# Optimization experiments

Measured on AMD Instinct MI355X. Metric: run time of the kernel, lower is better.

The kernel has to match this reference:

```python
import math
import jax, jax.numpy as jnp
import numpy as np

FACTOR = 5
HEAD_DIM = 64  # hard-coded in the original reshape


def setup_inputs() -> dict:
    key = jax.random.key(0)
    kq, kk, kv, ki = jax.random.split(key, 4)
    B, L, H, D = 16, 4096, 8, HEAD_DIM
    S = 4096
    u = FACTOR * math.ceil(math.log(L))  # sample_k = 45
    return {
        "queries": jax.random.normal(kq, (B, L, H, D), dtype=jnp.float32),
        "keys": jax.random.normal(kk, (B, S, H, D), dtype=jnp.float32),
        "values": jax.random.normal(kv, (B, S, H, D), dtype=jnp.float32),
        "sample_idx": jax.random.randint(ki, (u,), 0, S, dtype=jnp.int32),
    }


def reference(queries, keys, values, sample_idx):
    B, L, H, D = queries.shape
    S = keys.shape[1]
    # faithful to tf.reshape (memory reinterpret), not a transpose
    Q = queries.reshape(B, H, L, HEAD_DIM)
    K = keys.reshape(B, H, S, HEAD_DIM)
    V = values.reshape(B, H, S, HEAD_DIM)

    U = FACTOR * math.ceil(math.log(S))  # n_top queries kept

    # --- _prob_QK (without materializing K_expand: sampled keys are shared
    # across all query positions) ---
    K_sample = K[:, :, sample_idx, :]                      # [B,H,u,64]
    Q_K_sample = jnp.einsum('bhld,bhkd->bhlk', Q, K_sample)  # [B,H,L,u]
    # sparsity measure: max - mean (divided by full key length S)
    M = Q_K_sample.max(axis=-1) - Q_K_sample.sum(axis=-1) / S  # [B,H,L]
    _, M_top = jax.lax.top_k(M, U)                          # [B,H,U]

    Q_reduce = jnp.take_along_axis(Q, M_top[..., None], axis=2)  # [B,H,U,64]
    scores = jnp.einsum('bhud,bhsd->bhus', Q_reduce, K)          # [B,H,U,S]

    scale = 1.0 / math.sqrt(HEAD_DIM)
    scores = scores * scale

    # --- initial context: sum of V broadcast over all query positions ---
    V_sum = V.sum(axis=-2)                                  # [B,H,64]
    context = jnp.broadcast_to(V_sum[:, :, None, :], (B, H, L, HEAD_DIM))

    # --- update rows of the top-U queries with real attention output ---
    attn = jax.nn.softmax(scores, axis=-1)                  # [B,H,U,S]
    top_ctx = jnp.einsum('bhus,bhsd->bhud', attn, V)        # [B,H,U,64]

    b_idx = jnp.arange(B)[:, None, None]
    h_idx = jnp.arange(H)[None, :, None]
    context = context.at[b_idx, h_idx, M_top].set(top_ctx)
    return context
```

## Files before the change

### kernel.cpp

```cpp
#include <hip/hip_runtime.h>
#include <hip/hip_bf16.h>
#include <math.h>

#define NBH 128
#define LQ  4096
#define SK  4096
#define DH  64
#define NS  45
#define TOPSTRIDE 48
#define NCH 8
#define CK  512

typedef __attribute__((ext_vector_type(8))) short short8v;
typedef __attribute__((ext_vector_type(4))) short short4v;
typedef __attribute__((ext_vector_type(4))) float f32x4;

static __device__ __forceinline__ short f2b(float x) {
    union { __hip_bfloat16 h; short s; } u;
    u.h = __float2bfloat16(x);
    return u.s;
}
static __device__ __forceinline__ short8v cvt8(const float* p) {
    float4 a = *(const float4*)p, b = *(const float4*)(p + 4);
    short8v r;
    r[0]=f2b(a.x); r[1]=f2b(a.y); r[2]=f2b(a.z); r[3]=f2b(a.w);
    r[4]=f2b(b.x); r[5]=f2b(b.y); r[6]=f2b(b.z); r[7]=f2b(b.w);
    return r;
}
static __device__ __forceinline__ f32x4 mfma16(short4v a, short4v b, f32x4 c) {
#if __has_builtin(__builtin_amdgcn_mfma_f32_16x16x16bf16_1k)
    return __builtin_amdgcn_mfma_f32_16x16x16bf16_1k(a, b, c, 0, 0, 0);
#else
    asm volatile("v_mfma_f32_16x16x16_bf16 %0, %1, %2, %0" : "+v"(c) : "v"(a), "v"(b));
    return c;
#endif
}

__global__ __launch_bounds__(256) void kernelM(const float* __restrict__ Q,
                                               const float* __restrict__ K,
                                               const int* __restrict__ sidx,
                                               float* __restrict__ M) {
    __shared__ __attribute__((aligned(16))) float Ks[NS][DH];
    const int bh = blockIdx.x >> 4;
    const int qb = (blockIdx.x & 15) << 8;
    for (int i = threadIdx.x; i < NS * 16; i += 256) {
        int k = i >> 4, f4 = i & 15;
        *(float4*)&Ks[k][f4 * 4] =
            *(const float4*)(K + ((size_t)bh * SK + sidx[k]) * DH + f4 * 4);
    }
    __syncthreads();
    const int q = qb + threadIdx.x;
    const float* qp = Q + (((size_t)bh << 12) + q) * DH;
    float qr[DH];
#pragma unroll
    for (int i = 0; i < 16; i++) {
        float4 v = *(const float4*)(qp + 4 * i);
        qr[4*i] = v.x; qr[4*i+1] = v.y; qr[4*i+2] = v.z; qr[4*i+3] = v.w;
    }
    float vmax = -INFINITY, vsum = 0.f;
#pragma unroll 3
    for (int k = 0; k < NS; k++) {
        float d0 = 0.f, d1 = 0.f, d2 = 0.f, d3 = 0.f;
#pragma unroll
        for (int j = 0; j < 16; j++) {
            float4 kv = *(const float4*)&Ks[k][4 * j];
            d0 += qr[4*j+0] * kv.x;
            d1 += qr[4*j+1] * kv.y;
            d2 += qr[4*j+2] * kv.z;
            d3 += qr[4*j+3] * kv.w;
        }
        float dot = (d0 + d1) + (d2 + d3);
        vmax = fmaxf(vmax, dot);
        vsum += dot;
    }
    M[((size_t)bh << 12) + q] = vmax - vsum * (1.0f / 4096.0f);
}

__global__ __launch_bounds__(256) void kernelTopK(const float* __restrict__ M,
                                                  int* __restrict__ top) {
    __shared__ float m[LQ];
    __shared__ float rv[256];
    __shared__ int   ri[256];
    int bh = blockIdx.x;
    for (int i = threadIdx.x; i < LQ; i += 256) m[i] = M[((size_t)bh << 12) + i];
    __syncthreads();
    for (int it = 0; it < NS; ++it) {
        float bv = -INFINITY; int bi = 0x7fffffff;
        for (int i = threadIdx.x; i < LQ; i += 256) {
            float v = m[i];
            if (v > bv) { bv = v; bi = i; }
        }
        rv[threadIdx.x] = bv; ri[threadIdx.x] = bi;
        __syncthreads();
        for (int s = 128; s; s >>= 1) {
            if (threadIdx.x < s) {
                float ov = rv[threadIdx.x + s]; int oi = ri[threadIdx.x + s];
                if (ov > rv[threadIdx.x] || (ov == rv[threadIdx.x] && oi < ri[threadIdx.x])) {
                    rv[threadIdx.x] = ov; ri[threadIdx.x] = oi;
                }
            }
            __syncthreads();
        }
        if (threadIdx.x == 0) { top[bh * TOPSTRIDE + it] = ri[0]; m[ri[0]] = -INFINITY; }
        __syncthreads();
    }
}

__global__ __launch_bounds__(256) void kernelAttn2(const float* __restrict__ Q,
                                                   const float* __restrict__ K,
                                                   const float* __restrict__ V,
                                                   const int* __restrict__ top,
                                                   float* __restrict__ pm,
                                                   float* __restrict__ pl,
                                                   float* __restrict__ pacc,
                                                   float* __restrict__ vsum) {
    __shared__ float lm[4][48];
    __shared__ float ll[4][48];
    __shared__ __attribute__((aligned(16))) float ob[48][68];

    const int bh = blockIdx.x >> 3, c = blockIdx.x & 7;
    const int tid = threadIdx.x, w = tid >> 6, l = tid & 63;
    const int b = l >> 4, n = l & 15;
    const int kwavebase = c * CK + w * 128;
    const size_t bhoff = ((size_t)bh << 12) * DH;

    const int* topb = top + bh * TOPSTRIDE;
    short8v qf[3][2];
#pragma unroll
    for (int qt = 0; qt < 3; qt++) {
        int q = qt * 16 + n;
        int row = topb[q < NS ? q : NS - 1];
        const float* qp = Q + bhoff + (size_t)row * DH;
#pragma unroll
        for (int t = 0; t < 2; t++) qf[qt][t] = cvt8(qp + 32 * t + 8 * b);
    }

    f32x4 o[3][4];
    float m_run[3], l_run[3], vacc[4];
#pragma unroll
    for (int qt = 0; qt < 3; qt++) {
        m_run[qt] = -INFINITY; l_run[qt] = 0.f;
#pragma unroll
        for (int dt = 0; dt < 4; dt++) { o[qt][dt][0]=0.f; o[qt][dt][1]=0.f; o[qt][dt][2]=0.f; o[qt][dt][3]=0.f; }
    }
#pragma unroll
    for (int dt = 0; dt < 4; dt++) vacc[dt] = 0.f;

    for (int s = 0; s < 8; ++s) {
        const float* kp = K + bhoff + (size_t)(kwavebase + s * 16 + n) * DH;
        short8v ka0 = cvt8(kp + 8 * b);
        short8v ka1 = cvt8(kp + 32 + 8 * b);
        const float* vp = V + bhoff + (size_t)(kwavebase + s * 16 + 4 * b) * DH;
        short4v vb[4];
#pragma unroll
        for (int dt = 0; dt < 4; dt++) {
            float v0 = vp[0 * DH + dt * 16 + n];
            float v1 = vp[1 * DH + dt * 16 + n];
            float v2 = vp[2 * DH + dt * 16 + n];
            float v3 = vp[3 * DH + dt * 16 + n];
            vacc[dt] += (v0 + v1) + (v2 + v3);
            short4v vv; vv[0]=f2b(v0); vv[1]=f2b(v1); vv[2]=f2b(v2); vv[3]=f2b(v3);
            vb[dt] = vv;
        }
        f32x4 st[3];
        float mnew[3];
        bool need = false;
#pragma unroll
        for (int qt = 0; qt < 3; qt++) {
            f32x4 acc0 = {0.f, 0.f, 0.f, 0.f};
            acc0 = __builtin_amdgcn_mfma_f32_16x16x32_bf16(ka0, qf[qt][0], acc0, 0, 0, 0);
            acc0 = __builtin_amdgcn_mfma_f32_16x16x32_bf16(ka1, qf[qt][1], acc0, 0, 0, 0);
            acc0 = acc0 * 0.125f;
            st[qt] = acc0;
            float tm = fmaxf(fmaxf(acc0[0], acc0[1]), fmaxf(acc0[2], acc0[3]));
            tm = fmaxf(tm, __shfl_xor(tm, 16, 64));
            tm = fmaxf(tm, __shfl_xor(tm, 32, 64));
            mnew[qt] = fmaxf(m_run[qt], tm);
            need = need || (mnew[qt] > m_run[qt]);
        }
        if (__any(need)) {
            float rl[3];
#pragma unroll
            for (int qt = 0; qt < 3; qt++) {
                rl[qt] = __expf(m_run[qt] - mnew[qt]);
                l_run[qt] *= rl[qt];
            }
#pragma unroll
            for (int qt = 0; qt < 3; qt++) {
#pragma unroll
                for (int rr = 0; rr < 4; rr++) {
                    float rs = __shfl(rl[qt], 20 * b + rr, 64);
#pragma unroll
                    for (int dt = 0; dt < 4; dt++) o[qt][dt][rr] *= rs;
                }
            }
        }
#pragma unroll
        for (int qt = 0; qt < 3; qt++) {
            float p0 = __expf(st[qt][0] - mnew[qt]);
            float p1 = __expf(st[qt][1] - mnew[qt]);
            float p2 = __expf(st[qt][2] - mnew[qt]);
            float p3 = __expf(st[qt][3] - mnew[qt]);
            float ps = (p0 + p1) + (p2 + p3);
            ps += __shfl_xor(ps, 16, 64);
            ps += __shfl_xor(ps, 32, 64);
            l_run[qt] += ps;
            m_run[qt] = mnew[qt];
            short4v pa; pa[0]=f2b(p0); pa[1]=f2b(p1); pa[2]=f2b(p2); pa[3]=f2b(p3);
#pragma unroll
            for (int dt = 0; dt < 4; dt++) o[qt][dt] = mfma16(pa, vb[dt], o[qt][dt]);
        }
    }

    if (b == 0) {
#pragma unroll
        for (int qt = 0; qt < 3; qt++) lm[w][qt * 16 + n] = m_run[qt];
    }
    __syncthreads();
    float wf[3];
    {
        float mblk[3], lw[3];
#pragma unroll
        for (int qt = 0; qt < 3; qt++) {
            int q = qt * 16 + n;
            mblk[qt] = fmaxf(fmaxf(lm[0][q], lm[1][q]), fmaxf(lm[2][q], lm[3][q]));
            wf[qt] = __expf(m_run[qt] - mblk[qt]);
            lw[qt] = l_run[qt] * wf[qt];
        }
        if (b == 0) {
#pragma unroll
            for (int qt = 0; qt < 3; qt++) ll[w][qt * 16 + n] = lw[qt];
        }
        if (w == 0 && b == 0) {
#pragma unroll
            for (int qt = 0; qt < 3; qt++) {
                int q = qt * 16 + n;
                if (q < NS) pm[(size_t)(bh * NCH + c) * TOPSTRIDE + q] = mblk[qt];
            }
        }
    }
    float wsh[3][4];
#pragma unroll
    for (int qt = 0; qt < 3; qt++)
#pragma unroll
        for (int rr = 0; rr < 4; rr++) wsh[qt][rr] = __shfl(wf[qt], 20 * b + rr, 64);

    for (int ww = 0; ww < 4; ++ww) {
        if (w == ww) {
#pragma unroll
            for (int qt = 0; qt < 3; qt++)
#pragma unroll
                for (int dt = 0; dt < 4; dt++)
#pragma unroll
                    for (int rr = 0; rr < 4; rr++) {
                        int q = qt * 16 + 4 * b + rr, d = dt * 16 + n;
                        float val = o[qt][dt][rr] * wsh[qt][rr];
                        if (ww == 0) ob[q][d] = val; else ob[q][d] += val;
                    }
        }
        __syncthreads();
    }
    if (w == 0 && b == 0) {
#pragma unroll
        for (int qt = 0; qt < 3; qt++) {
            int q = qt * 16 + n;
            if (q < NS)
                pl[(size_t)(bh * NCH + c) * TOPSTRIDE + q] =
                    ((ll[0][q] + ll[1][q]) + (ll[2][q] + ll[3][q]));
        }
    }
    for (int i = tid; i < NS * 16; i += 256) {
        int q = i >> 4, f4 = i & 15;
        float4 v = *(const float4*)&ob[q][f4 * 4];
        *(float4*)&pacc[((size_t)(bh * NCH + c) * TOPSTRIDE + q) * DH + f4 * 4] = v;
    }
#pragma unroll
    for (int dt = 0; dt < 4; dt++) {
        float t = vacc[dt];
        t += __shfl_xor(t, 16, 64);
        t += __shfl_xor(t, 32, 64);
        if (b == 0) atomicAdd(vsum + bh * DH + dt * 16 + n, t);
    }
}

__global__ __launch_bounds__(256) void kernelBroadcast(const float* __restrict__ vsum,
                                                       float4* __restrict__ out4) {
    size_t i = (size_t)blockIdx.x * 256 + threadIdx.x;
    int bh = (int)(i >> 16);
    int d4 = (int)(i & 15);
    out4[i] = *(const float4*)(vsum + bh * DH + d4 * 4);
}

__global__ __launch_bounds__(256) void kernelCombine(const float* __restrict__ pm,
                                                     const float* __restrict__ pl,
                                                     const float* __restrict__ pacc,
                                                     const int* __restrict__ top,
                                                     float* __restrict__ out) {
    int g = (blockIdx.x << 2) | (threadIdx.x >> 6);
    int lane = threadIdx.x & 63;
    int bh = g / 45, u = g - bh * 45;
    float mc[NCH], lc[NCH];
    float mstar = -INFINITY;
#pragma unroll
    for (int c = 0; c < NCH; c++) {
        size_t pidx = ((size_t)bh * NCH + c) * TOPSTRIDE + u;
        mc[c] = pm[pidx]; lc[c] = pl[pidx];
        mstar = fmaxf(mstar, mc[c]);
    }
    float denom = 0.f, ctx = 0.f;
#pragma unroll
    for (int c = 0; c < NCH; c++) {
        size_t pidx = ((size_t)bh * NCH + c) * TOPSTRIDE + u;
        float wgt = __expf(mc[c] - mstar);
        denom += lc[c] * wgt;
        ctx += wgt * pacc[pidx * DH + lane];
    }
    int row = top[bh * TOPSTRIDE + u];
    out[(((size_t)bh << 12) + row) * DH + lane] = ctx / denom;
}

extern "C" void kernel_launch(void* const* d_in, const int* in_sizes, int n_in,
                              void* d_out, int out_size, void* d_ws, size_t ws_size,
                              hipStream_t stream) {
    const float* Q = (const float*)d_in[0];
    const float* K = (const float*)d_in[1];
    const float* V = (const float*)d_in[2];
    const int* sidx = (const int*)d_in[3];
    float* out = (float*)d_out;

    float* ws = (float*)d_ws;
    float* wsM    = ws;
    int*   wsTop  = (int*)(ws + 524288);
    float* wsVsum = ws + 524288 + 6144;
    float* wsPm   = wsVsum + 8192;
    float* wsPl   = wsPm + 49152;
    float* wsPacc = wsPl + 49152;

    hipMemsetAsync(wsVsum, 0, NBH * DH * sizeof(float), stream);
    kernelM<<<NBH * 16, 256, 0, stream>>>(Q, K, sidx, wsM);
    kernelTopK<<<NBH, 256, 0, stream>>>(wsM, wsTop);
    kernelAttn2<<<NBH * NCH, 256, 0, stream>>>(Q, K, V, wsTop, wsPm, wsPl, wsPacc, wsVsum);
    kernelBroadcast<<<32768, 256, 0, stream>>>(wsVsum, (float4*)out);
    kernelCombine<<<1440, 256, 0, stream>>>(wsPm, wsPl, wsPacc, wsTop, out);
}
```

Before: 541.0 us.

## Register-resident top-k with wave shuffles; read sampled keys via scalar loads

The top-k kernel keeps each thread's 16 M values and its running local max in registers. Each of the 45 selection rounds then does a wave shuffle reduction plus one cross-wave step through a double-buffered LDS array, replacing a full LDS rescan and an eight-step synchronised tree reduction. Only the thread that owned the winner recomputes its local max. The M kernel drops its LDS staging of the sampled keys and reads them through wave-uniform (readfirstlane) addresses so they become scalar/broadcast loads, accumulating 45 dot products in registers at the cost of higher register pressure.

```diff
diff --git a/kernel.cpp b/kernel.cpp
--- a/kernel.cpp
+++ b/kernel.cpp
@@ -40,69 +40,81 @@
                                                const float* __restrict__ K,
                                                const int* __restrict__ sidx,
                                                float* __restrict__ M) {
-    __shared__ __attribute__((aligned(16))) float Ks[NS][DH];
     const int bh = blockIdx.x >> 4;
-    const int qb = (blockIdx.x & 15) << 8;
-    for (int i = threadIdx.x; i < NS * 16; i += 256) {
-        int k = i >> 4, f4 = i & 15;
-        *(float4*)&Ks[k][f4 * 4] =
-            *(const float4*)(K + ((size_t)bh * SK + sidx[k]) * DH + f4 * 4);
-    }
-    __syncthreads();
-    const int q = qb + threadIdx.x;
+    const int q  = ((blockIdx.x & 15) << 8) + threadIdx.x;
     const float* qp = Q + (((size_t)bh << 12) + q) * DH;
-    float qr[DH];
-#pragma unroll
-    for (int i = 0; i < 16; i++) {
-        float4 v = *(const float4*)(qp + 4 * i);
-        qr[4*i] = v.x; qr[4*i+1] = v.y; qr[4*i+2] = v.z; qr[4*i+3] = v.w;
+    const size_t kbh = (size_t)bh * SK;
+    float dacc[NS];
+#pragma unroll
+    for (int k = 0; k < NS; k++) dacc[k] = 0.f;
+    for (int jt = 0; jt < 4; jt++) {
+        float4 q0 = *(const float4*)(qp + jt * 16);
+        float4 q1 = *(const float4*)(qp + jt * 16 + 4);
+        float4 q2 = *(const float4*)(qp + jt * 16 + 8);
+        float4 q3 = *(const float4*)(qp + jt * 16 + 12);
+#pragma unroll
+        for (int k = 0; k < NS; k++) {
+            int row = __builtin_amdgcn_readfirstlane(sidx[k]);
+            const float* kp = K + (kbh + row) * DH + jt * 16;
+            float d = dacc[k];
+            d = fmaf(q0.x, kp[0],  d); d = fmaf(q0.y, kp[1],  d);
+            d = fmaf(q0.z, kp[2],  d); d = fmaf(q0.w, kp[3],  d);
+            d = fmaf(q1.x, kp[4],  d); d = fmaf(q1.y, kp[5],  d);
+            d = fmaf(q1.z, kp[6],  d); d = fmaf(q1.w, kp[7],  d);
+            d = fmaf(q2.x, kp[8],  d); d = fmaf(q2.y, kp[9],  d);
+            d = fmaf(q2.z, kp[10], d); d = fmaf(q2.w, kp[11], d);
+            d = fmaf(q3.x, kp[12], d); d = fmaf(q3.y, kp[13], d);
+            d = fmaf(q3.z, kp[14], d); d = fmaf(q3.w, kp[15], d);
+            dacc[k] = d;
+        }
     }
     float vmax = -INFINITY, vsum = 0.f;
-#pragma unroll 3
-    for (int k = 0; k < NS; k++) {
-        float d0 = 0.f, d1 = 0.f, d2 = 0.f, d3 = 0.f;
-#pragma unroll
-        for (int j = 0; j < 16; j++) {
-            float4 kv = *(const float4*)&Ks[k][4 * j];
-            d0 += qr[4*j+0] * kv.x;
-            d1 += qr[4*j+1] * kv.y;
-            d2 += qr[4*j+2] * kv.z;
-            d3 += qr[4*j+3] * kv.w;
-        }
-        float dot = (d0 + d1) + (d2 + d3);
-        vmax = fmaxf(vmax, dot);
-        vsum += dot;
-    }
+#pragma unroll
+    for (int k = 0; k < NS; k++) { vmax = fmaxf(vmax, dacc[k]); vsum += dacc[k]; }
     M[((size_t)bh << 12) + q] = vmax - vsum * (1.0f / 4096.0f);
 }
 
 __global__ __launch_bounds__(256) void kernelTopK(const float* __restrict__ M,
                                                   int* __restrict__ top) {
-    __shared__ float m[LQ];
-    __shared__ float rv[256];
-    __shared__ int   ri[256];
-    int bh = blockIdx.x;
-    for (int i = threadIdx.x; i < LQ; i += 256) m[i] = M[((size_t)bh << 12) + i];
-    __syncthreads();
+    __shared__ float wv[2][4];
+    __shared__ int   wi[2][4];
+    const int bh = blockIdx.x, tid = threadIdx.x;
+    const int w = tid >> 6, l = tid & 63;
+    float mv[16];
+    float bv = -INFINITY; int bi = 0x7fffffff;
+#pragma unroll
+    for (int s = 0; s < 16; s++) {
+        mv[s] = M[((size_t)bh << 12) + tid + (s << 8)];
+        if (mv[s] > bv) { bv = mv[s]; bi = tid + (s << 8); }
+    }
     for (int it = 0; it < NS; ++it) {
-        float bv = -INFINITY; int bi = 0x7fffffff;
-        for (int i = threadIdx.x; i < LQ; i += 256) {
-            float v = m[i];
-            if (v > bv) { bv = v; bi = i; }
-        }
-        rv[threadIdx.x] = bv; ri[threadIdx.x] = bi;
+        float rv = bv; int ri = bi;
+#pragma unroll
+        for (int off = 1; off < 64; off <<= 1) {
+            float ov = __shfl_xor(rv, off, 64);
+            int   oi = __shfl_xor(ri, off, 64);
+            if (ov > rv || (ov == rv && oi < ri)) { rv = ov; ri = oi; }
+        }
+        const int buf = it & 1;
+        if (l == 0) { wv[buf][w] = rv; wi[buf][w] = ri; }
         __syncthreads();
-        for (int s = 128; s; s >>= 1) {
-            if (threadIdx.x < s) {
-                float ov = rv[threadIdx.x + s]; int oi = ri[threadIdx.x + s];
-                if (ov > rv[threadIdx.x] || (ov == rv[threadIdx.x] && oi < ri[threadIdx.x])) {
-                    rv[threadIdx.x] = ov; ri[threadIdx.x] = oi;
-                }
-            }
-            __syncthreads();
-        }
-        if (threadIdx.x == 0) { top[bh * TOPSTRIDE + it] = ri[0]; m[ri[0]] = -INFINITY; }
-        __syncthreads();
+        float fv = wv[buf][0]; int fi = wi[buf][0];
+#pragma unroll
+        for (int ww = 1; ww < 4; ww++) {
+            float ov = wv[buf][ww]; int oi = wi[buf][ww];
+            if (ov > fv || (ov == fv && oi < fi)) { fv = ov; fi = oi; }
+        }
+        if (tid == 0) top[bh * TOPSTRIDE + it] = fi;
+        if ((fi & 255) == tid) {
+            const int slot = fi >> 8;
+#pragma unroll
+            for (int s = 0; s < 16; s++)
+                if (s == slot) mv[s] = -INFINITY;
+            bv = -INFINITY; bi = 0x7fffffff;
+#pragma unroll
+            for (int s = 0; s < 16; s++)
+                if (mv[s] > bv) { bv = mv[s]; bi = tid + (s << 8); }
+        }
     }
 }
 
```

New measurement: 572.8 us. 5.9% more time.
